# Optimization experiments

Hardware: AMD Instinct MI355X
Metric: run time of the kernel (lower is better)

## Reference

```python
import jax, jax.numpy as jnp
import numpy as np

N_NODES = 50000
N_EDGES = 800000
D = 256
DEPTH = 10


def setup_inputs() -> dict:
    key = jax.random.key(0)
    ks = jax.random.split(key, 9)
    features = jax.random.normal(ks[0], (N_NODES, 6), dtype=jnp.float32)
    edge_src = jax.random.randint(ks[1], (N_EDGES,), 0, N_NODES, dtype=jnp.int32)
    edge_dst = jax.random.randint(ks[2], (N_EDGES,), 0, N_NODES, dtype=jnp.int32)
    s_in = 1.0 / np.sqrt(6.0)
    s_h = 1.0 / np.sqrt(D)
    W_in = jax.random.normal(ks[3], (6, D), dtype=jnp.float32) * s_in
    b_in = jax.random.normal(ks[4], (D,), dtype=jnp.float32) * s_in
    Ws = jax.random.normal(ks[5], (DEPTH, D, D), dtype=jnp.float32) * s_h
    bs = jax.random.normal(ks[6], (DEPTH, D), dtype=jnp.float32) * s_h
    W_out = jax.random.normal(ks[7], (D, 1), dtype=jnp.float32) * s_h
    b_out = jax.random.normal(ks[8], (1,), dtype=jnp.float32) * s_h
    return {"features": features, "edge_src": edge_src, "edge_dst": edge_dst,
            "W_in": W_in, "b_in": b_in, "Ws": Ws, "bs": bs,
            "W_out": W_out, "b_out": b_out}


def _gcn_layer(h, src, dst, W, b):
    # copy_src + sum: gather source features per edge, scatter-sum into dst nodes
    agg = jax.ops.segment_sum(h[src], dst, num_segments=N_NODES)  # [N, d_in]
    return agg @ W + b


def reference(features, edge_src, edge_dst, W_in, b_in, Ws, bs, W_out, b_out):
    x = jax.nn.relu(_gcn_layer(features, edge_src, edge_dst, W_in, b_in))

    def body(h, wb):
        W, b = wb
        return _gcn_layer(h, edge_src, edge_dst, W, b), None

    x, _ = jax.lax.scan(body, x, (Ws, bs))
    return _gcn_layer(x, edge_src, edge_dst, W_out, b_out)  # [N, 1]
```

## Files before the change

kernel.cpp:

```cpp
#include <hip/hip_runtime.h>
#include <hip/hip_bf16.h>

#define N_NODES 50000
#define N_EDGES 800000
#define D 256
#define DEPTH 10
#define PAD_CAP 48
#define SENTINEL 50000
#define EG ((N_EDGES + 255) / 256)


__global__ __launch_bounds__(256) void matvec_step_kernel(
    const float* __restrict__ W, const float* __restrict__ bsrow,
    const float* __restrict__ uin, float* __restrict__ uout,
    float* __restrict__ cout, int* __restrict__ cnt)
{
    const int b = blockIdx.x, t = threadIdx.x;
    if (b < 64) {
        const int wave = t >> 6, lane = t & 63;
        const int r = b * 4 + wave;
        float4 w4 = *reinterpret_cast<const float4*>(W + (size_t)r * D + lane * 4);
        float4 u4 = *reinterpret_cast<const float4*>(uin + lane * 4);
        float p = w4.x * u4.x + w4.y * u4.y + w4.z * u4.z + w4.w * u4.w;
        for (int off = 32; off > 0; off >>= 1) p += __shfl_down(p, off);
        if (lane == 0) uout[r] = p;
    } else if (b == 64) {
        if (t < 64) {
            float4 b4 = *reinterpret_cast<const float4*>(bsrow + t * 4);
            float4 u4 = *reinterpret_cast<const float4*>(uin + t * 4);
            float p = b4.x * u4.x + b4.y * u4.y + b4.z * u4.z + b4.w * u4.w;
            for (int off = 32; off > 0; off >>= 1) p += __shfl_down(p, off);
            if (t == 0) *cout = p;
        }
    } else {
        const int i = (b - 65) * 256 + t;
        if (i < N_NODES) cnt[i] = 0;
    }
}

__global__ __launch_bounds__(256) void scatter_pad_kernel(const int* __restrict__ src,
                                                          const int* __restrict__ dst,
                                                          int* __restrict__ cnt,
                                                          int* __restrict__ slots) {
    const int e = blockIdx.x * 256 + threadIdx.x;
    if (e >= N_EDGES) return;
    const int d = dst[e];
    const int pos = atomicAdd(&cnt[d], 1);
    if (pos < PAD_CAP) slots[(size_t)d * PAD_CAP + pos] = src[e];
}

__global__ __launch_bounds__(256) void y0_kernel(const float* __restrict__ feat,
                                                 const int* __restrict__ cnt,
                                                 int* __restrict__ slots,
                                                 const float* __restrict__ W_in,
                                                 const float* __restrict__ b_in,
                                                 const float* __restrict__ u0v,
                                                 float* __restrict__ ya,
                                                 float* __restrict__ yb) {
    __shared__ float Wsh[6 * D];
    __shared__ float bsh[D];
    __shared__ float ush[D];
    const int t = threadIdx.x;
    for (int i = t; i < 6 * D; i += 256) Wsh[i] = W_in[i];
    bsh[t] = b_in[t];
    ush[t] = u0v[t];
    __syncthreads();
    if (blockIdx.x == 0 && t < PAD_CAP) {
        ya[SENTINEL + t] = 0.f;
        yb[SENTINEL + t] = 0.f;
    }
    const int node = blockIdx.x * 256 + t;
    if (node >= N_NODES) return;
    int c = cnt[node]; if (c > PAD_CAP) c = PAD_CAP;
    int* sl = slots + (size_t)node * PAD_CAP;
    const int cr = (c + 3) & ~3;
    for (int i = c; i < cr; ++i) sl[i] = SENTINEL;
    float f0 = 0, f1 = 0, f2 = 0, f3 = 0, f4 = 0, f5 = 0;
    for (int jj = 0; jj < c; ++jj) {
        const float* fr = feat + (size_t)sl[jj] * 6;
        float2 a  = *reinterpret_cast<const float2*>(fr);
        float2 b2 = *reinterpret_cast<const float2*>(fr + 2);
        float2 cc = *reinterpret_cast<const float2*>(fr + 4);
        f0 += a.x; f1 += a.y; f2 += b2.x; f3 += b2.y; f4 += cc.x; f5 += cc.y;
    }
    float s = 0.f;
#pragma unroll 4
    for (int d2 = 0; d2 < D; ++d2) {
        float pre = bsh[d2]
                  + f0 * Wsh[d2]       + f1 * Wsh[256 + d2]  + f2 * Wsh[512 + d2]
                  + f3 * Wsh[768 + d2] + f4 * Wsh[1024 + d2] + f5 * Wsh[1280 + d2];
        s += fmaxf(pre, 0.f) * ush[d2];
    }
    ya[node] = s;
}

__global__ __launch_bounds__(256) void prop4_kernel(const float* __restrict__ yin,
                                                    float* __restrict__ yout,
                                                    const int* __restrict__ cnt,
                                                    const int* __restrict__ slots,
                                                    const float* __restrict__ cptr) {
    const int gid = blockIdx.x * 256 + threadIdx.x;
    const int node = gid >> 2, lane4 = gid & 3;
    if (node >= N_NODES) return;
    int c = cnt[node]; if (c > PAD_CAP) c = PAD_CAP;
    const int g4r = (c + 3) >> 2;
    const int4* sl = reinterpret_cast<const int4*>(slots + (size_t)node * PAD_CAP);
    float p = 0.f;
    for (int g = lane4; g < g4r; g += 4) {
        int4 v = sl[g];
        p += yin[v.x] + yin[v.y] + yin[v.z] + yin[v.w];
    }
    p += __shfl_xor(p, 1);
    p += __shfl_xor(p, 2);
    if (lane4 == 0) yout[node] = cptr[0] + p;
}


extern "C" void kernel_launch(void* const* d_in, const int* in_sizes, int n_in,
                              void* d_out, int out_size, void* d_ws, size_t ws_size,
                              hipStream_t stream) {
    const float* feat  = (const float*)d_in[0];
    const int*   src   = (const int*)d_in[1];
    const int*   dst   = (const int*)d_in[2];
    const float* W_in  = (const float*)d_in[3];
    const float* b_in  = (const float*)d_in[4];
    const float* Ws    = (const float*)d_in[5];
    const float* bsv   = (const float*)d_in[6];
    const float* W_out = (const float*)d_in[7];
    const float* b_out = (const float*)d_in[8];
    float* out = (float*)d_out;

    int*   cnt   = (int*)d_ws;
    int*   slots = cnt + 50048;
    float* uA    = (float*)(slots + (size_t)N_NODES * PAD_CAP);
    float* uB    = uA + 256;
    float* cbuf  = uB + 256;
    float* ya    = cbuf + 16;
    float* yb    = ya + 50048;

    const int B = 256;
    const int NG = (N_NODES + B - 1) / B;
    const int PG = (4 * N_NODES + B - 1) / B;

    {
        const float* uin = W_out;
        float* uout = uA;
        for (int s = 0; s < DEPTH; ++s) {
            const int j = DEPTH - s;
            const int grid = (s == 0) ? (65 + NG) : 65;
            matvec_step_kernel<<<grid, B, 0, stream>>>(
                Ws + (size_t)(j - 1) * D * D, bsv + (size_t)(j - 1) * D,
                uin, uout, cbuf + j, cnt);
            uin = uout;
            uout = (uout == uA) ? uB : uA;
        }
    }

    scatter_pad_kernel<<<EG, B, 0, stream>>>(src, dst, cnt, slots);

    y0_kernel<<<NG, B, 0, stream>>>(feat, cnt, slots, W_in, b_in, uB, ya, yb);

    float* cur = ya;
    float* nxt = yb;
    for (int k = 1; k <= DEPTH; ++k) {
        prop4_kernel<<<PG, B, 0, stream>>>(cur, nxt, cnt, slots, cbuf + k);
        float* tmp = cur; cur = nxt; nxt = tmp;
    }
    prop4_kernel<<<PG, B, 0, stream>>>(cur, out, cnt, slots, b_out);
}
```

Measured before the change: 167.4 us.

## Fuse ten matvec chain launches into one persistent kernel with grid barrier

Replaces the ten sequential matvec_step launches with a single kernel of 65 cooperating blocks that loop over the depth and sync through an atomic counter barrier in workspace. Intermediate u vectors pass between steps via agent-scope acquire/release atomics. The goal is to remove per-launch overhead on a tiny, latency-bound chain. It adds a memset launch and relies on all 65 chain blocks being co-resident, which the extra cnt-zeroing blocks in the same grid could in principle delay.

```diff
diff --git a/kernel.cpp b/kernel.cpp
--- a/kernel.cpp
+++ b/kernel.cpp
@@ -7,34 +7,63 @@
 #define DEPTH 10
 #define PAD_CAP 48
 #define SENTINEL 50000
+#define CHAIN_GRID 65
 #define EG ((N_EDGES + 255) / 256)
+#define NG ((N_NODES + 255) / 256)
 
 
-__global__ __launch_bounds__(256) void matvec_step_kernel(
-    const float* __restrict__ W, const float* __restrict__ bsrow,
-    const float* __restrict__ uin, float* __restrict__ uout,
-    float* __restrict__ cout, int* __restrict__ cnt)
+__global__ __launch_bounds__(256) void chain_fused_kernel(
+    const float* __restrict__ Ws, const float* __restrict__ bsv,
+    const float* __restrict__ W_out,
+    float* __restrict__ uA, float* __restrict__ uB, float* __restrict__ cbuf,
+    int* __restrict__ bar, int* __restrict__ cnt)
 {
     const int b = blockIdx.x, t = threadIdx.x;
-    if (b < 64) {
-        const int wave = t >> 6, lane = t & 63;
-        const int r = b * 4 + wave;
-        float4 w4 = *reinterpret_cast<const float4*>(W + (size_t)r * D + lane * 4);
-        float4 u4 = *reinterpret_cast<const float4*>(uin + lane * 4);
-        float p = w4.x * u4.x + w4.y * u4.y + w4.z * u4.z + w4.w * u4.w;
-        for (int off = 32; off > 0; off >>= 1) p += __shfl_down(p, off);
-        if (lane == 0) uout[r] = p;
-    } else if (b == 64) {
-        if (t < 64) {
-            float4 b4 = *reinterpret_cast<const float4*>(bsrow + t * 4);
-            float4 u4 = *reinterpret_cast<const float4*>(uin + t * 4);
-            float p = b4.x * u4.x + b4.y * u4.y + b4.z * u4.z + b4.w * u4.w;
+    if (b >= CHAIN_GRID) {
+        const int i = (b - CHAIN_GRID) * 256 + t;
+        if (i < N_NODES) cnt[i] = 0;
+        return;
+    }
+    const int wave = t >> 6, lane = t & 63;
+    for (int s = 0; s < DEPTH; ++s) {
+        const int j = DEPTH - s;
+        float u0, u1, u2, u3;
+        if (s == 0) {
+            const float* uin = W_out;
+            u0 = uin[lane * 4];     u1 = uin[lane * 4 + 1];
+            u2 = uin[lane * 4 + 2]; u3 = uin[lane * 4 + 3];
+        } else {
+            const float* uin = (s & 1) ? uA : uB;
+            u0 = __hip_atomic_load(uin + lane * 4,     __ATOMIC_ACQUIRE, __HIP_MEMORY_SCOPE_AGENT);
+            u1 = __hip_atomic_load(uin + lane * 4 + 1, __ATOMIC_ACQUIRE, __HIP_MEMORY_SCOPE_AGENT);
+            u2 = __hip_atomic_load(uin + lane * 4 + 2, __ATOMIC_ACQUIRE, __HIP_MEMORY_SCOPE_AGENT);
+            u3 = __hip_atomic_load(uin + lane * 4 + 3, __ATOMIC_ACQUIRE, __HIP_MEMORY_SCOPE_AGENT);
+        }
+        if (b < 64) {
+            const int r = b * 4 + wave;
+            float4 w4 = *reinterpret_cast<const float4*>(
+                Ws + (size_t)(j - 1) * D * D + (size_t)r * D + lane * 4);
+            float p = w4.x * u0 + w4.y * u1 + w4.z * u2 + w4.w * u3;
             for (int off = 32; off > 0; off >>= 1) p += __shfl_down(p, off);
-            if (t == 0) *cout = p;
+            float* uout = (s & 1) ? uB : uA;
+            if (lane == 0)
+                __hip_atomic_store(uout + r, p, __ATOMIC_RELEASE, __HIP_MEMORY_SCOPE_AGENT);
+        } else if (wave == 0) {
+            float4 b4 = *reinterpret_cast<const float4*>(
+                bsv + (size_t)(j - 1) * D + lane * 4);
+            float p = b4.x * u0 + b4.y * u1 + b4.z * u2 + b4.w * u3;
+            for (int off = 32; off > 0; off >>= 1) p += __shfl_down(p, off);
+            if (lane == 0) cbuf[j] = p;
         }
-    } else {
-        const int i = (b - 65) * 256 + t;
-        if (i < N_NODES) cnt[i] = 0;
+        if (s == DEPTH - 1) break;
+        __syncthreads();
+        if (t == 0) {
+            __hip_atomic_fetch_add(bar, 1, __ATOMIC_ACQ_REL, __HIP_MEMORY_SCOPE_AGENT);
+            const int target = CHAIN_GRID * (s + 1);
+            while (__hip_atomic_load(bar, __ATOMIC_ACQUIRE, __HIP_MEMORY_SCOPE_AGENT) < target)
+                __builtin_amdgcn_s_sleep(8);
+        }
+        __syncthreads();
     }
 }
 
@@ -135,26 +164,17 @@
     float* uA    = (float*)(slots + (size_t)N_NODES * PAD_CAP);
     float* uB    = uA + 256;
     float* cbuf  = uB + 256;
-    float* ya    = cbuf + 16;
+    int*   bar   = (int*)(cbuf + 16);
+    float* ya    = (float*)(bar + 64);
     float* yb    = ya + 50048;
 
     const int B = 256;
-    const int NG = (N_NODES + B - 1) / B;
     const int PG = (4 * N_NODES + B - 1) / B;
 
-    {
-        const float* uin = W_out;
-        float* uout = uA;
-        for (int s = 0; s < DEPTH; ++s) {
-            const int j = DEPTH - s;
-            const int grid = (s == 0) ? (65 + NG) : 65;
-            matvec_step_kernel<<<grid, B, 0, stream>>>(
-                Ws + (size_t)(j - 1) * D * D, bsv + (size_t)(j - 1) * D,
-                uin, uout, cbuf + j, cnt);
-            uin = uout;
-            uout = (uout == uA) ? uB : uA;
-        }
-    }
+    (void)hipMemsetAsync(bar, 0, 64 * 4, stream);
+
+    chain_fused_kernel<<<CHAIN_GRID + NG, B, 0, stream>>>(
+        Ws, bsv, W_out, uA, uB, cbuf, bar, cnt);
 
     scatter_pad_kernel<<<EG, B, 0, stream>>>(src, dst, cnt, slots);
 
```

Result: slower. 266.4 us (+59.1%).

## Fold edge scatter into matvec chain kernels split across nine chunks

Applied to the files above, without the earlier changes.

The standalone scatter kernel is removed. Its edge range is split into nine chunks, and each chunk runs as extra blocks of the nine later matvec-step launches. The tiny 65-block matvec launches, which otherwise leave the GPU idle, now carry useful scatter work, and one launch is saved. The trade-off is that the atomic scatter work is spread across serialized launches, and the s=0 launch still zeroes the counters first, so ordering stays correct.

```diff
diff --git a/kernel.cpp b/kernel.cpp
--- a/kernel.cpp
+++ b/kernel.cpp
@@ -7,13 +7,17 @@
 #define DEPTH 10
 #define PAD_CAP 48
 #define SENTINEL 50000
-#define EG ((N_EDGES + 255) / 256)
+#define NG ((N_NODES + 255) / 256)
+#define NCHUNK 9
+#define CHUNK_E ((N_EDGES + NCHUNK - 1) / NCHUNK)
+#define CHUNK_BLKS ((CHUNK_E + 255) / 256)
 
 
-__global__ __launch_bounds__(256) void matvec_step_kernel(
+__global__ __launch_bounds__(256) void combo_kernel(
     const float* __restrict__ W, const float* __restrict__ bsrow,
-    const float* __restrict__ uin, float* __restrict__ uout,
-    float* __restrict__ cout, int* __restrict__ cnt)
+    const float* __restrict__ uin, float* __restrict__ uout, float* __restrict__ cout,
+    int* __restrict__ cnt, const int* __restrict__ src, const int* __restrict__ dst,
+    int* __restrict__ slots, int ebase, int ecount)
 {
     const int b = blockIdx.x, t = threadIdx.x;
     if (b < 64) {
@@ -32,21 +36,17 @@
             for (int off = 32; off > 0; off >>= 1) p += __shfl_down(p, off);
             if (t == 0) *cout = p;
         }
-    } else {
+    } else if (ecount == 0) {
         const int i = (b - 65) * 256 + t;
         if (i < N_NODES) cnt[i] = 0;
+    } else {
+        const int e = ebase + (b - 65) * 256 + t;
+        if (e < ebase + ecount) {
+            const int d = dst[e];
+            const int pos = atomicAdd(&cnt[d], 1);
+            if (pos < PAD_CAP) slots[(size_t)d * PAD_CAP + pos] = src[e];
+        }
     }
-}
-
-__global__ __launch_bounds__(256) void scatter_pad_kernel(const int* __restrict__ src,
-                                                          const int* __restrict__ dst,
-                                                          int* __restrict__ cnt,
-                                                          int* __restrict__ slots) {
-    const int e = blockIdx.x * 256 + threadIdx.x;
-    if (e >= N_EDGES) return;
-    const int d = dst[e];
-    const int pos = atomicAdd(&cnt[d], 1);
-    if (pos < PAD_CAP) slots[(size_t)d * PAD_CAP + pos] = src[e];
 }
 
 __global__ __launch_bounds__(256) void y0_kernel(const float* __restrict__ feat,
@@ -139,24 +139,25 @@
     float* yb    = ya + 50048;
 
     const int B = 256;
-    const int NG = (N_NODES + B - 1) / B;
     const int PG = (4 * N_NODES + B - 1) / B;
 
     {
         const float* uin = W_out;
-        float* uout = uA;
         for (int s = 0; s < DEPTH; ++s) {
             const int j = DEPTH - s;
-            const int grid = (s == 0) ? (65 + NG) : 65;
-            matvec_step_kernel<<<grid, B, 0, stream>>>(
+            float* uout = (s & 1) ? uB : uA;
+            int ebase = 0, ecount = 0, grid = 65 + NG;
+            if (s >= 1) {
+                ebase  = (s - 1) * CHUNK_E;
+                ecount = (s == NCHUNK) ? (N_EDGES - ebase) : CHUNK_E;
+                grid   = 65 + CHUNK_BLKS;
+            }
+            combo_kernel<<<grid, B, 0, stream>>>(
                 Ws + (size_t)(j - 1) * D * D, bsv + (size_t)(j - 1) * D,
-                uin, uout, cbuf + j, cnt);
+                uin, uout, cbuf + j, cnt, src, dst, slots, ebase, ecount);
             uin = uout;
-            uout = (uout == uA) ? uB : uA;
         }
     }
-
-    scatter_pad_kernel<<<EG, B, 0, stream>>>(src, dst, cnt, slots);
 
     y0_kernel<<<NG, B, 0, stream>>>(feat, cnt, slots, W_in, b_in, uB, ya, yb);
 
```

Measured after the change: 160.0 us. 1.05x faster.
